# Kernel tuning notes

Measured on AMD Instinct MI355X. Metric: run time of the kernel, lower is better.

Reference implementation:

```python
import jax, jax.numpy as jnp
import numpy as np
import math

HEAD_DIM = 128
NUM_HEADS = 16
ROPE_BASE = 10000.0


def _rope(x, st_pos):
    # x: [B, S, H, hd], interleaved even/odd rotation as in the torch module
    S, hd = x.shape[1], x.shape[3]
    theta = 1.0 / (ROPE_BASE ** (jnp.arange(0, hd, 2, dtype=jnp.float32) / hd))  # [hd/2]
    pos = jnp.arange(st_pos, st_pos + S, dtype=jnp.float32)[:, None]             # [S,1]
    ang = pos * theta                                                            # [S, hd/2]
    sin = jnp.sin(ang)[None, :, None, :]
    cos = jnp.cos(ang)[None, :, None, :]
    xe, xo = x[..., 0::2], x[..., 1::2]
    re = xe * cos - xo * sin
    ro = xe * sin + xo * cos
    # re-interleave: stack pairs then flatten last two dims
    return jnp.stack([re, ro], axis=-1).reshape(x.shape)


def setup_inputs() -> dict:
    key = jax.random.key(0)
    ks = jax.random.split(key, 6)
    B, S, D = 4, 2048, 2048
    scale = 1.0 / math.sqrt(D)
    x = jax.random.normal(ks[0], (B, S, D), dtype=jnp.float32)
    # causal additive mask (prefill)
    mask = jnp.where(jnp.tril(jnp.ones((S, S), dtype=bool)), 0.0, -1e9).astype(jnp.float32)
    Wq = jax.random.normal(ks[1], (D, NUM_HEADS * HEAD_DIM), dtype=jnp.float32) * scale
    Wk = jax.random.normal(ks[2], (D, NUM_HEADS * HEAD_DIM), dtype=jnp.float32) * scale
    Wv = jax.random.normal(ks[3], (D, NUM_HEADS * HEAD_DIM), dtype=jnp.float32) * scale
    Wo = jax.random.normal(ks[4], (NUM_HEADS * HEAD_DIM, D), dtype=jnp.float32) * scale
    return {"x": x, "mask": mask, "Wq": Wq, "Wk": Wk, "Wv": Wv, "Wo": Wo, "st_pos": 0}


def reference(x, mask, Wq, Wk, Wv, Wo, st_pos):
    B, S, D = x.shape
    H, hd = NUM_HEADS, HEAD_DIM
    q = (x @ Wq).reshape(B, S, H, hd)
    k = (x @ Wk).reshape(B, S, H, hd)
    v = (x @ Wv).reshape(B, S, H, hd)
    q = _rope(q, st_pos)
    k = _rope(k, st_pos)
    # st_pos=0 prefill: cache slice == current k, v; n_rep == 1 (n_kv_heads=num_heads)
    scores = jnp.einsum('bqhd,bkhd->bhqk', q, k) / math.sqrt(hd)
    if mask is not None:
        scores = scores + mask
    attn = jax.nn.softmax(scores, axis=-1)
    a = jnp.einsum('bhqk,bkhd->bqhd', attn, v).reshape(B, S, H * hd)
    return a @ Wo
```

## Files before the change

kernel.cpp:

```cpp
#include <hip/hip_runtime.h>
#include <hip/hip_fp16.h>

typedef _Float16 f16;
typedef __attribute__((ext_vector_type(2))) _Float16 f16x2;
typedef __attribute__((ext_vector_type(4))) _Float16 f16x4v;
typedef __attribute__((ext_vector_type(8))) _Float16 f16x8;
typedef __attribute__((ext_vector_type(4))) float f32x4;
typedef __attribute__((ext_vector_type(4))) int i32x4;

#define DEV __device__ __forceinline__

static constexpr int S_ = 2048;
static constexpr int D_ = 2048;
static constexpr int H_ = 16;
static constexpr int HD_ = 128;
static constexpr int B_ = 4;

typedef const __attribute__((address_space(1))) void* gptr_t;
typedef __attribute__((address_space(3))) void* lptr_t;

DEV void gl_lds16(const void* gsrc, void* lds) {
  __builtin_amdgcn_global_load_lds((gptr_t)gsrc, (lptr_t)lds, 16, 0, 0);
}

DEV int cvt_pk_i32(float a, float b) {
  return __builtin_bit_cast(int, __builtin_amdgcn_cvt_pkrtz(a, b));
}

__global__ __launch_bounds__(256) void cvt_f32_to_f16(const float* __restrict__ in,
                                                      f16* __restrict__ out, long n) {
  long i0 = ((long)blockIdx.x * 256 + threadIdx.x) * 4;
  long stride = (long)gridDim.x * 256 * 4;
  for (long i = i0; i < n; i += stride) {
    float4 v = *(const float4*)(in + i);
    f16x4v o;
    o[0] = (f16)v.x; o[1] = (f16)v.y; o[2] = (f16)v.z; o[3] = (f16)v.w;
    *(f16x4v*)(out + i) = o;
  }
}

__global__ __launch_bounds__(256) void wtrans4(const float* __restrict__ W0, const float* __restrict__ W1,
                                               const float* __restrict__ W2, const float* __restrict__ W3,
                                               f16* __restrict__ Wt) {
  __shared__ float tile[32][33];
  int wi = blockIdx.y;
  const float* W = wi == 0 ? W0 : wi == 1 ? W1 : wi == 2 ? W2 : W3;
  f16* dst = Wt + (size_t)wi * D_ * D_;
  int bx = blockIdx.x & 63, by = blockIdx.x >> 6;
  int r0 = by << 5, c0 = bx << 5;
  int tx = threadIdx.x & 31, ty = threadIdx.x >> 5;
#pragma unroll
  for (int i = 0; i < 4; i++) {
    int r = ty + i * 8;
    tile[r][tx] = W[(size_t)(r0 + r) * D_ + c0 + tx];
  }
  __syncthreads();
#pragma unroll
  for (int i = 0; i < 4; i++) {
    int r = ty + i * 8;
    dst[(size_t)(c0 + r) * D_ + r0 + tx] = (f16)tile[tx][r];
  }
}

DEV f16x8 lds_frag(const f16* half, int row, int s, int lg) {
  int byte = row * 128 + s * 64 + lg * 16;
  byte ^= (row & 4) << 3;
  return *(const f16x8*)((const char*)half + byte);
}

template <typename CT>
__global__ __launch_bounds__(512, 2) void gemm8(const f16* __restrict__ A, const f16* __restrict__ Bt,
                                                CT* __restrict__ C, int M, int N, int K) {
  __shared__ alignas(16) f16 As[2][2][128 * 64];
  __shared__ alignas(16) f16 Bs[2][2][128 * 64];
  int nbx = N >> 8;
  int nwg = (M >> 8) * nbx;
  int bid = blockIdx.x;
  int wg = (bid & 7) * (nwg >> 3) + (bid >> 3);
  int bx = wg % nbx, by = wg / nbx;
  int tid = threadIdx.x, w = tid >> 6, l = tid & 63;
  int wm = w >> 2, wn = w & 3, lg = l >> 4, ln = l & 15;
  int nt = K >> 6;
  const f16* Ab = A + (size_t)(by * 256) * K;
  const f16* Bb = Bt + (size_t)(bx * 256) * K;

  auto stage = [&](const f16* src0, int kt, f16* dst) {
#pragma unroll
    for (int j = 0; j < 2; j++) {
      int c = j * 8 + w;
      int row = c * 8 + (l >> 3);
      int scol = ((l & 7) * 8) ^ ((row & 4) << 2);
      gl_lds16(src0 + (size_t)row * K + kt * 64 + scol, (char*)dst + c * 1024);
    }
  };

  f32x4 acc[8][4] = {};

  stage(Ab, 0, As[0][0]);
  stage(Ab + (size_t)128 * K, 0, As[0][1]);
  stage(Bb, 0, Bs[0][0]);
  stage(Bb + (size_t)128 * K, 0, Bs[0][1]);
  if (nt > 1) {
    stage(Bb, 1, Bs[1][0]);
    stage(Bb + (size_t)128 * K, 1, Bs[1][1]);
  }

  for (int t = 0; t < nt; t++) {
    if (t + 2 < nt) asm volatile("s_waitcnt vmcnt(4)" ::: "memory");
    else            asm volatile("s_waitcnt vmcnt(0)" ::: "memory");
    __builtin_amdgcn_s_barrier();
    asm volatile("" ::: "memory");
    const f16* Ah = As[t & 1][wm];
    const f16* Bh = Bs[t & 1][wn >> 1];
    int br0 = (wn & 1) * 64;
    f16x8 a[4], b0[4], b1[4];
#pragma unroll
    for (int i = 0; i < 4; i++) a[i] = lds_frag(Ah, i * 16 + ln, 0, lg);
#pragma unroll
    for (int i = 0; i < 4; i++) b0[i] = lds_frag(Bh, br0 + i * 16 + ln, 0, lg);
    if (t + 1 < nt) stage(Ab, t + 1, As[(t + 1) & 1][0]);
    __builtin_amdgcn_s_barrier();
    asm volatile("" ::: "memory");
    __builtin_amdgcn_s_setprio(1);
#pragma unroll
    for (int mi = 0; mi < 4; mi++)
#pragma unroll
      for (int ni = 0; ni < 4; ni++)
        acc[mi][ni] = __builtin_amdgcn_mfma_f32_16x16x32_f16(a[mi], b0[ni], acc[mi][ni], 0, 0, 0);
    __builtin_amdgcn_s_setprio(0);
    __builtin_amdgcn_s_barrier();
    asm volatile("" ::: "memory");
#pragma unroll
    for (int i = 0; i < 4; i++) a[i] = lds_frag(Ah, i * 16 + ln, 1, lg);
#pragma unroll
    for (int i = 0; i < 4; i++) b1[i] = lds_frag(Bh, br0 + i * 16 + ln, 1, lg);
    if (t + 1 < nt) stage(Ab + (size_t)128 * K, t + 1, As[(t + 1) & 1][1]);
    __builtin_amdgcn_s_barrier();
    asm volatile("" ::: "memory");
    __builtin_amdgcn_s_setprio(1);
#pragma unroll
    for (int mi = 0; mi < 4; mi++)
#pragma unroll
      for (int ni = 0; ni < 4; ni++)
        acc[mi][ni] = __builtin_amdgcn_mfma_f32_16x16x32_f16(a[mi], b1[ni], acc[mi][ni], 0, 0, 0);
    __builtin_amdgcn_s_setprio(0);
    __builtin_amdgcn_s_barrier();
    asm volatile("" ::: "memory");
#pragma unroll
    for (int i = 0; i < 4; i++) a[i] = lds_frag(Ah, 64 + i * 16 + ln, 0, lg);
    if (t + 2 < nt) stage(Bb, t + 2, Bs[t & 1][0]);
    __builtin_amdgcn_s_barrier();
    asm volatile("" ::: "memory");
    __builtin_amdgcn_s_setprio(1);
#pragma unroll
    for (int mi = 0; mi < 4; mi++)
#pragma unroll
      for (int ni = 0; ni < 4; ni++)
        acc[mi + 4][ni] = __builtin_amdgcn_mfma_f32_16x16x32_f16(a[mi], b0[ni], acc[mi + 4][ni], 0, 0, 0);
    __builtin_amdgcn_s_setprio(0);
    __builtin_amdgcn_s_barrier();
    asm volatile("" ::: "memory");
#pragma unroll
    for (int i = 0; i < 4; i++) a[i] = lds_frag(Ah, 64 + i * 16 + ln, 1, lg);
    if (t + 2 < nt) stage(Bb + (size_t)128 * K, t + 2, Bs[t & 1][1]);
    __builtin_amdgcn_s_barrier();
    asm volatile("" ::: "memory");
    __builtin_amdgcn_s_setprio(1);
#pragma unroll
    for (int mi = 0; mi < 4; mi++)
#pragma unroll
      for (int ni = 0; ni < 4; ni++)
        acc[mi + 4][ni] = __builtin_amdgcn_mfma_f32_16x16x32_f16(a[mi], b1[ni], acc[mi + 4][ni], 0, 0, 0);
    __builtin_amdgcn_s_setprio(0);
    __builtin_amdgcn_s_barrier();
    asm volatile("" ::: "memory");
  }

  int row0 = by * 256 + wm * 128;
  int col0 = bx * 256 + wn * 64;
#pragma unroll
  for (int mi = 0; mi < 8; mi++)
#pragma unroll
    for (int ni = 0; ni < 4; ni++)
#pragma unroll
      for (int r4 = 0; r4 < 4; r4++) {
        int row = row0 + mi * 16 + lg * 4 + r4;
        int col = col0 + ni * 16 + ln;
        float o = acc[mi][ni][r4];
        if constexpr (sizeof(CT) == 2) {
          float oo = __shfl_xor(o, 1);
          if (!(ln & 1)) {
            f16x2 pp; pp[0] = (f16)o; pp[1] = (f16)oo;
            *(f16x2*)(&C[(size_t)row * N + col]) = pp;
          }
        } else {
          C[(size_t)row * N + col] = o;
        }
      }
}

__global__ __launch_bounds__(256) void rope_table(float2* __restrict__ tab, const int* __restrict__ st) {
  int i = blockIdx.x * 256 + threadIdx.x;
  int s = i >> 6, j = i & 63;
  float theta = powf(10000.f, -(float)j / 64.f);
  float ang = (float)(s + st[0]) * theta;
  tab[i] = make_float2(cosf(ang), sinf(ang));
}

__global__ __launch_bounds__(256) void rope_apply(f16* __restrict__ X, const float2* __restrict__ tab,
                                                  float scale, long npairs) {
  long i0 = (long)blockIdx.x * 256 + threadIdx.x;
  long stride = (long)gridDim.x * 256;
  for (long p = i0; p < npairs; p += stride) {
    long row = p >> 10;
    int jp = (int)(p & 1023);
    int s = (int)(row & (S_ - 1));
    float2 cs = tab[s * 64 + (jp & 63)];
    f16x2 v = *(const f16x2*)(X + 2 * p);
    float xe = (float)v[0], xo = (float)v[1];
    float re = (xe * cs.x - xo * cs.y) * scale;
    float ro = (xe * cs.y + xo * cs.x) * scale;
    f16x2 o; o[0] = (f16)re; o[1] = (f16)ro;
    *(f16x2*)(X + 2 * p) = o;
  }
}

__global__ __launch_bounds__(256) void vtrans2(const f16* __restrict__ V, f16* __restrict__ VT2) {
  __shared__ alignas(16) f16 tile[64 * 128];
  int t = blockIdx.x, bh = blockIdx.y, b = bh >> 4, h = bh & 15;
  int tid = threadIdx.x, w = tid >> 6, l = tid & 63, lg = l >> 4, ln = l & 15;
  const f16* src = V + ((size_t)(b * S_ + t * 64) * H_ + h) * HD_;
#pragma unroll
  for (int i = 0; i < 4; i++) {
    int idx = i * 256 + tid;
    int r = idx >> 4, c8 = idx & 15;
    int c8s = c8 ^ ((r >> 3) & 3);
    *(f16x8*)(&tile[r * 128 + c8s * 8]) = *(const f16x8*)(src + (size_t)r * (H_ * HD_) + c8 * 8);
  }
  __syncthreads();
  f16* dst = VT2 + (size_t)(bh * 32 + t) * 16 * 512;
#pragma unroll
  for (int ci = 0; ci < 4; ci++) {
    int c = w * 4 + ci;
    int nj = c >> 1, kk = c & 1;
    f16x8 v;
#pragma unroll
    for (int e = 0; e < 8; e++) {
      int r = 16 * (2 * kk + (e >> 2)) + 4 * lg + (e & 3);
      int col = nj * 16 + ln;
      int c8s = (col >> 3) ^ ((r >> 3) & 3);
      v[e] = tile[r * 128 + c8s * 8 + (col & 7)];
    }
    *(f16x8*)(dst + (size_t)c * 512 + l * 8) = v;
  }
}

__global__ __launch_bounds__(512, 4) void attn(const f16* __restrict__ Q, const f16* __restrict__ K,
                                               const f16* __restrict__ VT2, f16* __restrict__ O,
                                               const float2* __restrict__ tab) {
  __shared__ alignas(16) f16 kls[2][64 * 128];
  int id = blockIdx.x;
  int r8 = id & 7, j = id >> 3;
  int u = j & 7, g = j >> 3;
  int bh = r8 + (g << 3);
  int b = bh >> 4, h = bh & 15;
  int tid = threadIdx.x, w = tid >> 6, l = tid & 63, lg = l >> 4, ln = l & 15;

  const float QSCALE = 0.12751744910173355f;
  const f16* kp = K + (size_t)(b * S_) * D_ + h * HD_;
  const f16* vp2 = VT2 + (size_t)bh * 32 * 16 * 512;

  auto stageK = [&](int buf, int kv0) {
#pragma unroll
    for (int jj = 0; jj < 2; jj++) {
      int i = jj * 8 + w;
      int byte = i * 1024 + 16 * l;
      int r = byte >> 8;
      int c = (((byte >> 4) & 15) - r) & 15;
      gl_lds16(kp + (size_t)(kv0 + r) * D_ + c * 8, (char*)kls[buf] + i * 1024);
    }
  };

#pragma unroll 1
  for (int pi = 0; pi < 2; pi++) {
    int qsel = pi ? u : 15 - u;
    int q0 = qsel << 7;
    int qrow = q0 + w * 16 + ln;
    const f16* qp = Q + (size_t)(b * S_ + qrow) * D_ + h * HD_;
    const float2* tq = tab + (size_t)qrow * 64;
    f16x8 qf[4];
#pragma unroll
    for (int kc = 0; kc < 4; kc++) {
      f16x8 q = *(const f16x8*)(qp + kc * 32 + lg * 8);
#pragma unroll
      for (int p = 0; p < 4; p++) {
        float2 cs = tq[kc * 16 + lg * 4 + p];
        float e0 = (float)q[2 * p], e1 = (float)q[2 * p + 1];
        q[2 * p] = (f16)((e0 * cs.x - e1 * cs.y) * QSCALE);
        q[2 * p + 1] = (f16)((e0 * cs.y + e1 * cs.x) * QSCALE);
      }
      qf[kc] = q;
    }

    float m = -1e30f, lsum = 0.f;
    f32x4 oacc[8] = {};

    int nt = (q0 >> 6) + 2;
    if (pi) __syncthreads();
    stageK(0, 0);
    for (int t = 0; t < nt; t++) {
      int kv0 = t << 6;
      int cur = t & 1;
      __syncthreads();
      if (t + 1 < nt) stageK(cur ^ 1, (t + 1) << 6);
      if (kv0 > q0 + w * 16 + 15) continue;
      const f16* kb = kls[cur];
      const f16* vt = vp2 + (size_t)t * 16 * 512;

      f32x4 sf[4];
      __builtin_amdgcn_s_setprio(1);
#pragma unroll
      for (int ni = 0; ni < 4; ni++) {
        int n = ni * 16 + ln;
        f32x4 s = {0.f, 0.f, 0.f, 0.f};
#pragma unroll
        for (int kc = 0; kc < 4; kc++) {
          int mch = kc * 4 + lg;
          f16x8 kf = *(const f16x8*)(&kb[n * 128 + (((mch + n) & 15) << 3)]);
          s = __builtin_amdgcn_mfma_f32_16x16x32_f16(kf, qf[kc], s, 0, 0, 0);
        }
        sf[ni] = s;
      }
      __builtin_amdgcn_s_setprio(0);

      f16x8 vfa[8];
#pragma unroll
      for (int c = 0; c < 8; c++) vfa[c] = *(const f16x8*)(vt + c * 512 + l * 8);

      if (t >= nt - 2) {
#pragma unroll
        for (int ni = 0; ni < 4; ni++) {
          int kvg = kv0 + ni * 16 + lg * 4;
#pragma unroll
          for (int r4 = 0; r4 < 4; r4++)
            if (kvg + r4 > qrow) sf[ni][r4] = -1e30f;
        }
      }
      float pm = fmaxf(fmaxf(fmaxf(sf[0][0], sf[0][1]), fmaxf(sf[0][2], sf[0][3])),
                       fmaxf(fmaxf(sf[1][0], sf[1][1]), fmaxf(sf[1][2], sf[1][3])));
      pm = fmaxf(pm, fmaxf(fmaxf(fmaxf(sf[2][0], sf[2][1]), fmaxf(sf[2][2], sf[2][3])),
                           fmaxf(fmaxf(sf[3][0], sf[3][1]), fmaxf(sf[3][2], sf[3][3]))));
      pm = fmaxf(pm, __shfl_xor(pm, 16));
      pm = fmaxf(pm, __shfl_xor(pm, 32));
      float scl = 1.f;
      bool defer = __all(pm <= m + 8.f);
      if (!defer) {
        float mn = fmaxf(m, pm);
        scl = __builtin_amdgcn_exp2f(m - mn);
        m = mn;
      }
      float rsum = 0.f;
#pragma unroll
      for (int ni = 0; ni < 4; ni++)
#pragma unroll
        for (int r4 = 0; r4 < 4; r4++) {
          float p = __builtin_amdgcn_exp2f(sf[ni][r4] - m);
          sf[ni][r4] = p;
          rsum += p;
        }
      lsum = lsum * scl + rsum;

      if (!defer) {
#pragma unroll
        for (int nj = 0; nj < 8; nj++)
#pragma unroll
          for (int r4 = 0; r4 < 4; r4++) oacc[nj][r4] *= scl;
      }

      f16x8 pa[2];
#pragma unroll
      for (int kk = 0; kk < 2; kk++) {
        i32x4 wv;
        wv.x = cvt_pk_i32(sf[2 * kk][0], sf[2 * kk][1]);
        wv.y = cvt_pk_i32(sf[2 * kk][2], sf[2 * kk][3]);
        wv.z = cvt_pk_i32(sf[2 * kk + 1][0], sf[2 * kk + 1][1]);
        wv.w = cvt_pk_i32(sf[2 * kk + 1][2], sf[2 * kk + 1][3]);
        pa[kk] = __builtin_bit_cast(f16x8, wv);
      }

      __builtin_amdgcn_s_setprio(1);
#pragma unroll
      for (int kk = 0; kk < 2; kk++)
#pragma unroll
        for (int nj = 0; nj < 4; nj++)
          oacc[nj] = __builtin_amdgcn_mfma_f32_16x16x32_f16(vfa[nj * 2 + kk], pa[kk], oacc[nj], 0, 0, 0);
#pragma unroll
      for (int njb = 0; njb < 2; njb++) {
        f16x8 vf[4];
#pragma unroll
        for (int jj = 0; jj < 2; jj++)
#pragma unroll
          for (int kk = 0; kk < 2; kk++)
            vf[jj * 2 + kk] = *(const f16x8*)(vt + (size_t)(((4 + njb * 2 + jj) * 2 + kk) * 512) + l * 8);
#pragma unroll
        for (int kk = 0; kk < 2; kk++)
#pragma unroll
          for (int jj = 0; jj < 2; jj++)
            oacc[4 + njb * 2 + jj] = __builtin_amdgcn_mfma_f32_16x16x32_f16(
                vf[jj * 2 + kk], pa[kk], oacc[4 + njb * 2 + jj], 0, 0, 0);
      }
      __builtin_amdgcn_s_setprio(0);
    }

    lsum += __shfl_xor(lsum, 16);
    lsum += __shfl_xor(lsum, 32);
    f16* op = O + (size_t)(b * S_ + qrow) * D_ + h * HD_;
    float inv = 1.f / lsum;
#pragma unroll
    for (int nj = 0; nj < 8; nj++) {
      f16x4v ov;
#pragma unroll
      for (int r4 = 0; r4 < 4; r4++) ov[r4] = (f16)(oacc[nj][r4] * inv);
      *(f16x4v*)(op + nj * 16 + lg * 4) = ov;
    }
  }
}

extern "C" void kernel_launch(void* const* d_in, const int* in_sizes, int n_in,
                              void* d_out, int out_size, void* d_ws, size_t ws_size,
                              hipStream_t stream) {
  (void)in_sizes; (void)n_in; (void)out_size; (void)ws_size;
  const float* x = (const float*)d_in[0];
  const float* Wq = (const float*)d_in[2];
  const float* Wk = (const float*)d_in[3];
  const float* Wv = (const float*)d_in[4];
  const float* Wo = (const float*)d_in[5];
  const int* stp = (const int*)d_in[6];
  float* out = (float*)d_out;

  const size_t MS = (size_t)B_ * S_;
  f16* xh = (f16*)d_ws;
  f16* wqt = xh + MS * D_;
  f16* wkt = wqt + (size_t)D_ * D_;
  f16* wvt = wkt + (size_t)D_ * D_;
  f16* wot = wvt + (size_t)D_ * D_;
  f16* qh = wot + (size_t)D_ * D_;
  f16* kh = qh + MS * D_;
  f16* vh = kh + MS * D_;
  float2* tab = (float2*)(vh + MS * D_);
  f16* vt2 = xh;
  f16* aoh = vh;

  cvt_f32_to_f16<<<16384, 256, 0, stream>>>(x, xh, (long)(MS * D_));
  wtrans4<<<dim3(4096, 4), 256, 0, stream>>>(Wq, Wk, Wv, Wo, wqt);
  gemm8<f16><<<256, 512, 0, stream>>>(xh, wqt, qh, 8192, 2048, 2048);
  gemm8<f16><<<256, 512, 0, stream>>>(xh, wkt, kh, 8192, 2048, 2048);
  gemm8<f16><<<256, 512, 0, stream>>>(xh, wvt, vh, 8192, 2048, 2048);
  rope_table<<<512, 256, 0, stream>>>(tab, stp);
  rope_apply<<<4096, 256, 0, stream>>>(kh, tab, 1.0f, (long)(MS * 1024));
  vtrans2<<<dim3(32, 64), 256, 0, stream>>>(vh, vt2);
  attn<<<512, 512, 0, stream>>>(qh, kh, vt2, aoh, tab);
  gemm8<float><<<256, 512, 0, stream>>>(aoh, wot, out, 8192, 2048, 2048);
}
```

Baseline: 467.2 us.

## Fuse Q/K/V projections into one GEMM with interleaved QKV layout

Replaces three separate Q, K, V projection GEMMs with a single GEMM over concatenated weights, writing an interleaved [rows, 6144] QKV buffer. Rope, V transpose, attention and the output GEMM now read from strided QKV rows, and the output GEMM gains an lda parameter. Attention now double-buffers two 64-row K tiles per sync, halving the number of barriers, and writes its output in place over Q. The aim is fewer launches, better GEMM occupancy and fewer barriers in attention, at the cost of doubled LDS use in attention and strided, less compact K/V reads.

```diff
diff --git a/kernel.cpp b/kernel.cpp
--- a/kernel.cpp
+++ b/kernel.cpp
@@ -15,6 +15,7 @@
 static constexpr int H_ = 16;
 static constexpr int HD_ = 128;
 static constexpr int B_ = 4;
+static constexpr int QKV_ST = 6144;
 
 typedef const __attribute__((address_space(1))) void* gptr_t;
 typedef __attribute__((address_space(3))) void* lptr_t;
@@ -70,7 +71,7 @@
 
 template <typename CT>
 __global__ __launch_bounds__(512, 2) void gemm8(const f16* __restrict__ A, const f16* __restrict__ Bt,
-                                                CT* __restrict__ C, int M, int N, int K) {
+                                                CT* __restrict__ C, int M, int N, int K, int lda) {
   __shared__ alignas(16) f16 As[2][2][128 * 64];
   __shared__ alignas(16) f16 Bs[2][2][128 * 64];
   int nbx = N >> 8;
@@ -81,10 +82,19 @@
   int tid = threadIdx.x, w = tid >> 6, l = tid & 63;
   int wm = w >> 2, wn = w & 3, lg = l >> 4, ln = l & 15;
   int nt = K >> 6;
-  const f16* Ab = A + (size_t)(by * 256) * K;
+  const f16* Ab = A + (size_t)(by * 256) * lda;
   const f16* Bb = Bt + (size_t)(bx * 256) * K;
 
-  auto stage = [&](const f16* src0, int kt, f16* dst) {
+  auto stageA = [&](const f16* src0, int kt, f16* dst) {
+#pragma unroll
+    for (int j = 0; j < 2; j++) {
+      int c = j * 8 + w;
+      int row = c * 8 + (l >> 3);
+      int scol = ((l & 7) * 8) ^ ((row & 4) << 2);
+      gl_lds16(src0 + (size_t)row * lda + kt * 64 + scol, (char*)dst + c * 1024);
+    }
+  };
+  auto stageB = [&](const f16* src0, int kt, f16* dst) {
 #pragma unroll
     for (int j = 0; j < 2; j++) {
       int c = j * 8 + w;
@@ -96,13 +106,13 @@
 
   f32x4 acc[8][4] = {};
 
-  stage(Ab, 0, As[0][0]);
-  stage(Ab + (size_t)128 * K, 0, As[0][1]);
-  stage(Bb, 0, Bs[0][0]);
-  stage(Bb + (size_t)128 * K, 0, Bs[0][1]);
+  stageA(Ab, 0, As[0][0]);
+  stageA(Ab + (size_t)128 * lda, 0, As[0][1]);
+  stageB(Bb, 0, Bs[0][0]);
+  stageB(Bb + (size_t)128 * K, 0, Bs[0][1]);
   if (nt > 1) {
-    stage(Bb, 1, Bs[1][0]);
-    stage(Bb + (size_t)128 * K, 1, Bs[1][1]);
+    stageB(Bb, 1, Bs[1][0]);
+    stageB(Bb + (size_t)128 * K, 1, Bs[1][1]);
   }
 
   for (int t = 0; t < nt; t++) {
@@ -118,7 +128,7 @@
     for (int i = 0; i < 4; i++) a[i] = lds_frag(Ah, i * 16 + ln, 0, lg);
 #pragma unroll
     for (int i = 0; i < 4; i++) b0[i] = lds_frag(Bh, br0 + i * 16 + ln, 0, lg);
-    if (t + 1 < nt) stage(Ab, t + 1, As[(t + 1) & 1][0]);
+    if (t + 1 < nt) stageA(Ab, t + 1, As[(t + 1) & 1][0]);
     __builtin_amdgcn_s_barrier();
     asm volatile("" ::: "memory");
     __builtin_amdgcn_s_setprio(1);
@@ -134,7 +144,7 @@
     for (int i = 0; i < 4; i++) a[i] = lds_frag(Ah, i * 16 + ln, 1, lg);
 #pragma unroll
     for (int i = 0; i < 4; i++) b1[i] = lds_frag(Bh, br0 + i * 16 + ln, 1, lg);
-    if (t + 1 < nt) stage(Ab + (size_t)128 * K, t + 1, As[(t + 1) & 1][1]);
+    if (t + 1 < nt) stageA(Ab + (size_t)128 * lda, t + 1, As[(t + 1) & 1][1]);
     __builtin_amdgcn_s_barrier();
     asm volatile("" ::: "memory");
     __builtin_amdgcn_s_setprio(1);
@@ -148,7 +158,7 @@
     asm volatile("" ::: "memory");
 #pragma unroll
     for (int i = 0; i < 4; i++) a[i] = lds_frag(Ah, 64 + i * 16 + ln, 0, lg);
-    if (t + 2 < nt) stage(Bb, t + 2, Bs[t & 1][0]);
+    if (t + 2 < nt) stageB(Bb, t + 2, Bs[t & 1][0]);
     __builtin_amdgcn_s_barrier();
     asm volatile("" ::: "memory");
     __builtin_amdgcn_s_setprio(1);
@@ -162,7 +172,7 @@
     asm volatile("" ::: "memory");
 #pragma unroll
     for (int i = 0; i < 4; i++) a[i] = lds_frag(Ah, 64 + i * 16 + ln, 1, lg);
-    if (t + 2 < nt) stage(Bb + (size_t)128 * K, t + 2, Bs[t & 1][1]);
+    if (t + 2 < nt) stageB(Bb + (size_t)128 * K, t + 2, Bs[t & 1][1]);
     __builtin_amdgcn_s_barrier();
     asm volatile("" ::: "memory");
     __builtin_amdgcn_s_setprio(1);
@@ -207,8 +217,8 @@
   tab[i] = make_float2(cosf(ang), sinf(ang));
 }
 
-__global__ __launch_bounds__(256) void rope_apply(f16* __restrict__ X, const float2* __restrict__ tab,
-                                                  float scale, long npairs) {
+__global__ __launch_bounds__(256) void rope_apply_k(f16* __restrict__ QKV, const float2* __restrict__ tab,
+                                                    long npairs) {
   long i0 = (long)blockIdx.x * 256 + threadIdx.x;
   long stride = (long)gridDim.x * 256;
   for (long p = i0; p < npairs; p += stride) {
@@ -216,26 +226,27 @@
     int jp = (int)(p & 1023);
     int s = (int)(row & (S_ - 1));
     float2 cs = tab[s * 64 + (jp & 63)];
-    f16x2 v = *(const f16x2*)(X + 2 * p);
+    f16* px = QKV + row * QKV_ST + 2048 + 2 * jp;
+    f16x2 v = *(const f16x2*)px;
     float xe = (float)v[0], xo = (float)v[1];
-    float re = (xe * cs.x - xo * cs.y) * scale;
-    float ro = (xe * cs.y + xo * cs.x) * scale;
+    float re = xe * cs.x - xo * cs.y;
+    float ro = xe * cs.y + xo * cs.x;
     f16x2 o; o[0] = (f16)re; o[1] = (f16)ro;
-    *(f16x2*)(X + 2 * p) = o;
-  }
-}
-
-__global__ __launch_bounds__(256) void vtrans2(const f16* __restrict__ V, f16* __restrict__ VT2) {
+    *(f16x2*)px = o;
+  }
+}
+
+__global__ __launch_bounds__(256) void vtrans2(const f16* __restrict__ QKV, f16* __restrict__ VT2) {
   __shared__ alignas(16) f16 tile[64 * 128];
   int t = blockIdx.x, bh = blockIdx.y, b = bh >> 4, h = bh & 15;
   int tid = threadIdx.x, w = tid >> 6, l = tid & 63, lg = l >> 4, ln = l & 15;
-  const f16* src = V + ((size_t)(b * S_ + t * 64) * H_ + h) * HD_;
+  const f16* src = QKV + (size_t)(b * S_ + t * 64) * QKV_ST + 4096 + h * HD_;
 #pragma unroll
   for (int i = 0; i < 4; i++) {
     int idx = i * 256 + tid;
     int r = idx >> 4, c8 = idx & 15;
     int c8s = c8 ^ ((r >> 3) & 3);
-    *(f16x8*)(&tile[r * 128 + c8s * 8]) = *(const f16x8*)(src + (size_t)r * (H_ * HD_) + c8 * 8);
+    *(f16x8*)(&tile[r * 128 + c8s * 8]) = *(const f16x8*)(src + (size_t)r * QKV_ST + c8 * 8);
   }
   __syncthreads();
   f16* dst = VT2 + (size_t)(bh * 32 + t) * 16 * 512;
@@ -255,10 +266,9 @@
   }
 }
 
-__global__ __launch_bounds__(512, 4) void attn(const f16* __restrict__ Q, const f16* __restrict__ K,
-                                               const f16* __restrict__ VT2, f16* __restrict__ O,
+__global__ __launch_bounds__(512, 4) void attn(f16* __restrict__ QKV, const f16* __restrict__ VT2,
                                                const float2* __restrict__ tab) {
-  __shared__ alignas(16) f16 kls[2][64 * 128];
+  __shared__ alignas(16) f16 kls[2][2][64 * 128];
   int id = blockIdx.x;
   int r8 = id & 7, j = id >> 3;
   int u = j & 7, g = j >> 3;
@@ -267,17 +277,17 @@
   int tid = threadIdx.x, w = tid >> 6, l = tid & 63, lg = l >> 4, ln = l & 15;
 
   const float QSCALE = 0.12751744910173355f;
-  const f16* kp = K + (size_t)(b * S_) * D_ + h * HD_;
+  const f16* kp = QKV + (size_t)(b * S_) * QKV_ST + 2048 + h * HD_;
   const f16* vp2 = VT2 + (size_t)bh * 32 * 16 * 512;
 
-  auto stageK = [&](int buf, int kv0) {
+  auto stageK = [&](int buf, int half, int kv0) {
 #pragma unroll
     for (int jj = 0; jj < 2; jj++) {
       int i = jj * 8 + w;
       int byte = i * 1024 + 16 * l;
       int r = byte >> 8;
       int c = (((byte >> 4) & 15) - r) & 15;
-      gl_lds16(kp + (size_t)(kv0 + r) * D_ + c * 8, (char*)kls[buf] + i * 1024);
+      gl_lds16(kp + (size_t)(kv0 + r) * QKV_ST + c * 8, (char*)kls[buf][half] + i * 1024);
     }
   };
 
@@ -286,7 +296,7 @@
     int qsel = pi ? u : 15 - u;
     int q0 = qsel << 7;
     int qrow = q0 + w * 16 + ln;
-    const f16* qp = Q + (size_t)(b * S_ + qrow) * D_ + h * HD_;
+    f16* qp = QKV + (size_t)(b * S_ + qrow) * QKV_ST + h * HD_;
     const float2* tq = tab + (size_t)qrow * 64;
     f16x8 qf[4];
 #pragma unroll
@@ -305,123 +315,131 @@
     float m = -1e30f, lsum = 0.f;
     f32x4 oacc[8] = {};
 
-    int nt = (q0 >> 6) + 2;
+    int np = qsel + 1;
+    int nt64 = 2 * qsel + 2;
     if (pi) __syncthreads();
-    stageK(0, 0);
-    for (int t = 0; t < nt; t++) {
-      int kv0 = t << 6;
-      int cur = t & 1;
+    stageK(0, 0, 0);
+    stageK(0, 1, 64);
+#pragma unroll 1
+    for (int p = 0; p < np; p++) {
       __syncthreads();
-      if (t + 1 < nt) stageK(cur ^ 1, (t + 1) << 6);
-      if (kv0 > q0 + w * 16 + 15) continue;
-      const f16* kb = kls[cur];
-      const f16* vt = vp2 + (size_t)t * 16 * 512;
-
-      f32x4 sf[4];
-      __builtin_amdgcn_s_setprio(1);
-#pragma unroll
-      for (int ni = 0; ni < 4; ni++) {
-        int n = ni * 16 + ln;
-        f32x4 s = {0.f, 0.f, 0.f, 0.f};
-#pragma unroll
-        for (int kc = 0; kc < 4; kc++) {
-          int mch = kc * 4 + lg;
-          f16x8 kf = *(const f16x8*)(&kb[n * 128 + (((mch + n) & 15) << 3)]);
-          s = __builtin_amdgcn_mfma_f32_16x16x32_f16(kf, qf[kc], s, 0, 0, 0);
-        }
-        sf[ni] = s;
+      if (p + 1 < np) {
+        stageK((p + 1) & 1, 0, (2 * p + 2) << 6);
+        stageK((p + 1) & 1, 1, (2 * p + 3) << 6);
       }
-      __builtin_amdgcn_s_setprio(0);
-
-      f16x8 vfa[8];
-#pragma unroll
-      for (int c = 0; c < 8; c++) vfa[c] = *(const f16x8*)(vt + c * 512 + l * 8);
-
-      if (t >= nt - 2) {
+#pragma unroll 1
+      for (int ii = 0; ii < 2; ii++) {
+        int t = 2 * p + ii;
+        int kv0 = t << 6;
+        if (kv0 > q0 + w * 16 + 15) continue;
+        const f16* kb = kls[p & 1][ii];
+        const f16* vt = vp2 + (size_t)t * 16 * 512;
+
+        f32x4 sf[4];
+        __builtin_amdgcn_s_setprio(1);
 #pragma unroll
         for (int ni = 0; ni < 4; ni++) {
-          int kvg = kv0 + ni * 16 + lg * 4;
-#pragma unroll
-          for (int r4 = 0; r4 < 4; r4++)
-            if (kvg + r4 > qrow) sf[ni][r4] = -1e30f;
-        }
+          int n = ni * 16 + ln;
+          f32x4 s = {0.f, 0.f, 0.f, 0.f};
+#pragma unroll
+          for (int kc = 0; kc < 4; kc++) {
+            int mch = kc * 4 + lg;
+            f16x8 kf = *(const f16x8*)(&kb[n * 128 + (((mch + n) & 15) << 3)]);
+            s = __builtin_amdgcn_mfma_f32_16x16x32_f16(kf, qf[kc], s, 0, 0, 0);
+          }
+          sf[ni] = s;
+        }
+        __builtin_amdgcn_s_setprio(0);
+
+        f16x8 vfa[8];
+#pragma unroll
+        for (int c = 0; c < 8; c++) vfa[c] = *(const f16x8*)(vt + c * 512 + l * 8);
+
+        if (t >= nt64 - 2) {
+#pragma unroll
+          for (int ni = 0; ni < 4; ni++) {
+            int kvg = kv0 + ni * 16 + lg * 4;
+#pragma unroll
+            for (int r4 = 0; r4 < 4; r4++)
+              if (kvg + r4 > qrow) sf[ni][r4] = -1e30f;
+          }
+        }
+        float pm = fmaxf(fmaxf(fmaxf(sf[0][0], sf[0][1]), fmaxf(sf[0][2], sf[0][3])),
+                         fmaxf(fmaxf(sf[1][0], sf[1][1]), fmaxf(sf[1][2], sf[1][3])));
+        pm = fmaxf(pm, fmaxf(fmaxf(fmaxf(sf[2][0], sf[2][1]), fmaxf(sf[2][2], sf[2][3])),
+                             fmaxf(fmaxf(sf[3][0], sf[3][1]), fmaxf(sf[3][2], sf[3][3]))));
+        pm = fmaxf(pm, __shfl_xor(pm, 16));
+        pm = fmaxf(pm, __shfl_xor(pm, 32));
+        float scl = 1.f;
+        bool defer = __all(pm <= m + 8.f);
+        if (!defer) {
+          float mn = fmaxf(m, pm);
+          scl = __builtin_amdgcn_exp2f(m - mn);
+          m = mn;
+        }
+        float rsum = 0.f;
+#pragma unroll
+        for (int ni = 0; ni < 4; ni++)
+#pragma unroll
+          for (int r4 = 0; r4 < 4; r4++) {
+            float pv = __builtin_amdgcn_exp2f(sf[ni][r4] - m);
+            sf[ni][r4] = pv;
+            rsum += pv;
+          }
+        lsum = lsum * scl + rsum;
+
+        if (!defer) {
+#pragma unroll
+          for (int nj = 0; nj < 8; nj++)
+#pragma unroll
+            for (int r4 = 0; r4 < 4; r4++) oacc[nj][r4] *= scl;
+        }
+
+        f16x8 pa[2];
+#pragma unroll
+        for (int kk = 0; kk < 2; kk++) {
+          i32x4 wv;
+          wv.x = cvt_pk_i32(sf[2 * kk][0], sf[2 * kk][1]);
+          wv.y = cvt_pk_i32(sf[2 * kk][2], sf[2 * kk][3]);
+          wv.z = cvt_pk_i32(sf[2 * kk + 1][0], sf[2 * kk + 1][1]);
+          wv.w = cvt_pk_i32(sf[2 * kk + 1][2], sf[2 * kk + 1][3]);
+          pa[kk] = __builtin_bit_cast(f16x8, wv);
+        }
+
+        __builtin_amdgcn_s_setprio(1);
+#pragma unroll
+        for (int kk = 0; kk < 2; kk++)
+#pragma unroll
+          for (int nj = 0; nj < 4; nj++)
+            oacc[nj] = __builtin_amdgcn_mfma_f32_16x16x32_f16(vfa[nj * 2 + kk], pa[kk], oacc[nj], 0, 0, 0);
+#pragma unroll
+        for (int njb = 0; njb < 2; njb++) {
+          f16x8 vf[4];
+#pragma unroll
+          for (int jj = 0; jj < 2; jj++)
+#pragma unroll
+            for (int kk = 0; kk < 2; kk++)
+              vf[jj * 2 + kk] = *(const f16x8*)(vt + (size_t)(((4 + njb * 2 + jj) * 2 + kk) * 512) + l * 8);
+#pragma unroll
+          for (int kk = 0; kk < 2; kk++)
+#pragma unroll
+            for (int jj = 0; jj < 2; jj++)
+              oacc[4 + njb * 2 + jj] = __builtin_amdgcn_mfma_f32_16x16x32_f16(
+                  vf[jj * 2 + kk], pa[kk], oacc[4 + njb * 2 + jj], 0, 0, 0);
+        }
+        __builtin_amdgcn_s_setprio(0);
       }
-      float pm = fmaxf(fmaxf(fmaxf(sf[0][0], sf[0][1]), fmaxf(sf[0][2], sf[0][3])),
-                       fmaxf(fmaxf(sf[1][0], sf[1][1]), fmaxf(sf[1][2], sf[1][3])));
-      pm = fmaxf(pm, fmaxf(fmaxf(fmaxf(sf[2][0], sf[2][1]), fmaxf(sf[2][2], sf[2][3])),
-                           fmaxf(fmaxf(sf[3][0], sf[3][1]), fmaxf(sf[3][2], sf[3][3]))));
-      pm = fmaxf(pm, __shfl_xor(pm, 16));
-      pm = fmaxf(pm, __shfl_xor(pm, 32));
-      float scl = 1.f;
-      bool defer = __all(pm <= m + 8.f);
-      if (!defer) {
-        float mn = fmaxf(m, pm);
-        scl = __builtin_amdgcn_exp2f(m - mn);
-        m = mn;
-      }
-      float rsum = 0.f;
-#pragma unroll
-      for (int ni = 0; ni < 4; ni++)
-#pragma unroll
-        for (int r4 = 0; r4 < 4; r4++) {
-          float p = __builtin_amdgcn_exp2f(sf[ni][r4] - m);
-          sf[ni][r4] = p;
-          rsum += p;
-        }
-      lsum = lsum * scl + rsum;
-
-      if (!defer) {
-#pragma unroll
-        for (int nj = 0; nj < 8; nj++)
-#pragma unroll
-          for (int r4 = 0; r4 < 4; r4++) oacc[nj][r4] *= scl;
-      }
-
-      f16x8 pa[2];
-#pragma unroll
-      for (int kk = 0; kk < 2; kk++) {
-        i32x4 wv;
-        wv.x = cvt_pk_i32(sf[2 * kk][0], sf[2 * kk][1]);
-        wv.y = cvt_pk_i32(sf[2 * kk][2], sf[2 * kk][3]);
-        wv.z = cvt_pk_i32(sf[2 * kk + 1][0], sf[2 * kk + 1][1]);
-        wv.w = cvt_pk_i32(sf[2 * kk + 1][2], sf[2 * kk + 1][3]);
-        pa[kk] = __builtin_bit_cast(f16x8, wv);
-      }
-
-      __builtin_amdgcn_s_setprio(1);
-#pragma unroll
-      for (int kk = 0; kk < 2; kk++)
-#pragma unroll
-        for (int nj = 0; nj < 4; nj++)
-          oacc[nj] = __builtin_amdgcn_mfma_f32_16x16x32_f16(vfa[nj * 2 + kk], pa[kk], oacc[nj], 0, 0, 0);
-#pragma unroll
-      for (int njb = 0; njb < 2; njb++) {
-        f16x8 vf[4];
-#pragma unroll
-        for (int jj = 0; jj < 2; jj++)
-#pragma unroll
-          for (int kk = 0; kk < 2; kk++)
-            vf[jj * 2 + kk] = *(const f16x8*)(vt + (size_t)(((4 + njb * 2 + jj) * 2 + kk) * 512) + l * 8);
-#pragma unroll
-        for (int kk = 0; kk < 2; kk++)
-#pragma unroll
-          for (int jj = 0; jj < 2; jj++)
-            oacc[4 + njb * 2 + jj] = __builtin_amdgcn_mfma_f32_16x16x32_f16(
-                vf[jj * 2 + kk], pa[kk], oacc[4 + njb * 2 + jj], 0, 0, 0);
-      }
-      __builtin_amdgcn_s_setprio(0);
     }
 
     lsum += __shfl_xor(lsum, 16);
     lsum += __shfl_xor(lsum, 32);
-    f16* op = O + (size_t)(b * S_ + qrow) * D_ + h * HD_;
     float inv = 1.f / lsum;
 #pragma unroll
     for (int nj = 0; nj < 8; nj++) {
       f16x4v ov;
 #pragma unroll
       for (int r4 = 0; r4 < 4; r4++) ov[r4] = (f16)(oacc[nj][r4] * inv);
-      *(f16x4v*)(op + nj * 16 + lg * 4) = ov;
+      *(f16x4v*)(qp + nj * 16 + lg * 4) = ov;
     }
   }
 }
@@ -441,24 +459,17 @@
   const size_t MS = (size_t)B_ * S_;
   f16* xh = (f16*)d_ws;
   f16* wqt = xh + MS * D_;
-  f16* wkt = wqt + (size_t)D_ * D_;
-  f16* wvt = wkt + (size_t)D_ * D_;
-  f16* wot = wvt + (size_t)D_ * D_;
-  f16* qh = wot + (size_t)D_ * D_;
-  f16* kh = qh + MS * D_;
-  f16* vh = kh + MS * D_;
-  float2* tab = (float2*)(vh + MS * D_);
+  f16* wot = wqt + (size_t)3 * D_ * D_;
+  f16* qkv = wqt + (size_t)4 * D_ * D_;
+  float2* tab = (float2*)(qkv + MS * (size_t)QKV_ST);
   f16* vt2 = xh;
-  f16* aoh = vh;
 
   cvt_f32_to_f16<<<16384, 256, 0, stream>>>(x, xh, (long)(MS * D_));
   wtrans4<<<dim3(4096, 4), 256, 0, stream>>>(Wq, Wk, Wv, Wo, wqt);
-  gemm8<f16><<<256, 512, 0, stream>>>(xh, wqt, qh, 8192, 2048, 2048);
-  gemm8<f16><<<256, 512, 0, stream>>>(xh, wkt, kh, 8192, 2048, 2048);
-  gemm8<f16><<<256, 512, 0, stream>>>(xh, wvt, vh, 8192, 2048, 2048);
+  gemm8<f16><<<768, 512, 0, stream>>>(xh, wqt, qkv, 8192, 6144, 2048, 2048);
   rope_table<<<512, 256, 0, stream>>>(tab, stp);
-  rope_apply<<<4096, 256, 0, stream>>>(kh, tab, 1.0f, (long)(MS * 1024));
-  vtrans2<<<dim3(32, 64), 256, 0, stream>>>(vh, vt2);
-  attn<<<512, 512, 0, stream>>>(qh, kh, vt2, aoh, tab);
-  gemm8<float><<<256, 512, 0, stream>>>(aoh, wot, out, 8192, 2048, 2048);
-}
+  rope_apply_k<<<4096, 256, 0, stream>>>(qkv, tab, (long)(MS * 1024));
+  vtrans2<<<dim3(32, 64), 256, 0, stream>>>(qkv, vt2);
+  attn<<<512, 512, 0, stream>>>(qkv, vt2, tab);
+  gemm8<float><<<256, 512, 0, stream>>>(qkv, wot, out, 8192, 2048, 2048, QKV_ST);
+}
```

New measurement: 466.9 us. Within noise of the previous version (-0.1%).
